# Performance work log

Hardware: AMD Instinct MI355X
Metric: run time of the kernel (lower is better)

Reference implementation:

```python
import jax, jax.numpy as jnp
import numpy as np

B, S, D = 2, 1024, 1024          # batch, seq_len, d_model
L, H = 512, 16                   # latent_d_model, num_heads
HD = L // H                      # latent head dim = 32
F, E, K = 2048, 8, 2             # d_ff per expert, num_experts, top_k
THETA = 10000.0
EPS = 1e-5


def setup_inputs() -> dict:
    key = jax.random.key(0)
    ks = jax.random.split(key, 12)
    g = lambda k, shape, scale: jax.random.normal(k, shape, dtype=jnp.float32) * scale
    return {
        "x": g(ks[0], (B, S, D), 1.0),
        "g1": jnp.ones((D,), jnp.float32),
        "g2": jnp.ones((D,), jnp.float32),
        "w_down": g(ks[1], (D, L), 0.02),   # latent down-projection
        "wq": g(ks[2], (L, L), 0.02),
        "wk": g(ks[3], (L, L), 0.02),
        "wv": g(ks[4], (L, L), 0.02),
        "w_up": g(ks[5], (L, D), 0.02),     # output up-projection
        "router_w": g(ks[6], (D, E), 0.02),
        "w1": g(ks[7], (E, D, F), 0.02),    # SwiGLU gate proj per expert
        "w3": g(ks[8], (E, D, F), 0.02),    # SwiGLU up proj per expert
        "w2": g(ks[9], (E, F, D), 0.02),    # SwiGLU down proj per expert
    }


def _rmsnorm(x, g):
    return x * g * jax.lax.rsqrt(jnp.mean(x * x, axis=-1, keepdims=True) + EPS)


def _rope(t, pos):
    # t: [B, H, S, HD]; RoPE on interleaved pairs of the compressed-latent heads
    inv_freq = 1.0 / (THETA ** (jnp.arange(0, HD, 2, dtype=jnp.float32) / HD))  # [HD/2]
    ang = pos[:, None].astype(jnp.float32) * inv_freq[None, :]                  # [S, HD/2]
    cos, sin = jnp.cos(ang), jnp.sin(ang)
    t1, t2 = t[..., 0::2], t[..., 1::2]
    r1 = t1 * cos - t2 * sin
    r2 = t1 * sin + t2 * cos
    return jnp.stack([r1, r2], axis=-1).reshape(t.shape)


def _forward(x, g1, g2, w_down, wq, wk, wv, w_up, router_w, w1, w2, w3):
    b, s, _ = x.shape
    pos = jnp.arange(s)

    # --- MLA (latent multi-head self-attention with RoPE) ---
    h = _rmsnorm(x, g1)
    c = h @ w_down                                        # [b,s,L] compressed latent
    split = lambda t: t.reshape(b, s, H, HD).transpose(0, 2, 1, 3)
    q = _rope(split(c @ wq), pos)
    k = _rope(split(c @ wk), pos)
    v = split(c @ wv)
    scores = jnp.einsum("bhqd,bhkd->bhqk", q, k) / jnp.sqrt(jnp.float32(HD))
    causal = jnp.tril(jnp.ones((s, s), bool))
    scores = jnp.where(causal, scores, -jnp.inf)
    attn = jax.nn.softmax(scores, axis=-1)
    o = jnp.einsum("bhqk,bhkd->bhqd", attn, v).transpose(0, 2, 1, 3).reshape(b, s, L)
    x = x + o @ w_up

    # --- Switch MoE FFN (top-k routing, SwiGLU experts) ---
    res = x
    t = _rmsnorm(x, g2).reshape(-1, D)                    # [T,D]
    probs = jax.nn.softmax(t @ router_w, axis=-1)         # [T,E]
    vals, idx = jax.lax.top_k(probs, K)                   # [T,K]
    w = vals / jnp.sum(vals, axis=-1, keepdims=True)      # renormalized gates
    gate = jnp.sum(jax.nn.one_hot(idx, E, dtype=t.dtype) * w[..., None], axis=1)  # [T,E]
    hid = jax.nn.silu(jnp.einsum("td,edf->tef", t, w1)) * jnp.einsum("td,edf->tef", t, w3)
    y_e = jnp.einsum("tef,efd->ted", hid, w2)             # per-expert outputs
    y = jnp.einsum("ted,te->td", y_e, gate)
    return res + y.reshape(b, s, D)


def reference(x, g1, g2, w_down, wq, wk, wv, w_up, router_w, w1, w2, w3):
    return _forward(x, g1, g2, w_down, wq, wk, wv, w_up, router_w, w1, w2, w3)
```

## Files before the change

kernel.cpp:

```cpp
#include <hip/hip_runtime.h>

#define Bb 2
#define Ss 1024
#define Dd 1024
#define Ll 512
#define Hh 16
#define HDd 32
#define Ff 2048
#define Ee 8
#define Tt 2048
#define EPSf 1e-5f
#define THETAf 10000.0f

typedef unsigned short u16;
typedef unsigned int u32;
typedef short s16x8 __attribute__((ext_vector_type(8)));
typedef float f32x4 __attribute__((ext_vector_type(4)));

__device__ __forceinline__ float bf2f(u16 u) {
    union { u32 i; float f; } v; v.i = ((u32)u) << 16; return v.f;
}
__device__ __forceinline__ u16 f2bf(float f) {
    union { float f; u32 i; } v; v.f = f;
    u32 u = v.i;
    u32 r = (u + 0x7FFFu + ((u >> 16) & 1u)) >> 16;
    return (u16)r;
}

__global__ __launch_bounds__(256) void rmsnorm1_k(const float* __restrict__ x,
                                                  const float* __restrict__ g,
                                                  u16* __restrict__ hhi,
                                                  u16* __restrict__ hlo) {
    int row = blockIdx.x, tid = threadIdx.x;
    __shared__ float red[256];
    float xv[4]; float ss = 0.f;
    #pragma unroll
    for (int i = 0; i < 4; i++) {
        int d = tid + i * 256;
        xv[i] = x[(size_t)row * Dd + d];
        ss += xv[i] * xv[i];
    }
    red[tid] = ss; __syncthreads();
    for (int s2 = 128; s2 > 0; s2 >>= 1) {
        if (tid < s2) red[tid] += red[tid + s2];
        __syncthreads();
    }
    float scale = rsqrtf(red[0] / (float)Dd + EPSf);
    #pragma unroll
    for (int i = 0; i < 4; i++) {
        int d = tid + i * 256;
        float h = xv[i] * g[d] * scale;
        u16 hi = f2bf(h);
        hhi[(size_t)row * Dd + d] = hi;
        hlo[(size_t)row * Dd + d] = f2bf(h - bf2f(hi));
    }
}

__global__ __launch_bounds__(256) void rmsnorm2_router_k(
    const float* __restrict__ x2, const float* __restrict__ g,
    const float* __restrict__ rw, u16* __restrict__ t2h,
    float* __restrict__ gate_w, int* __restrict__ counts,
    int* __restrict__ list_tok, int* __restrict__ list_gid) {
    int row = blockIdx.x, tid = threadIdx.x;
    __shared__ float red[256];
    __shared__ float pw[4][8];
    float xv[4]; float ss = 0.f;
    #pragma unroll
    for (int i = 0; i < 4; i++) {
        int d = tid + i * 256;
        xv[i] = x2[(size_t)row * Dd + d];
        ss += xv[i] * xv[i];
    }
    red[tid] = ss; __syncthreads();
    for (int s2 = 128; s2 > 0; s2 >>= 1) {
        if (tid < s2) red[tid] += red[tid + s2];
        __syncthreads();
    }
    float scale = rsqrtf(red[0] / (float)Dd + EPSf);
    float pl[Ee];
    #pragma unroll
    for (int e = 0; e < Ee; e++) pl[e] = 0.f;
    #pragma unroll
    for (int i = 0; i < 4; i++) {
        int d = tid + i * 256;
        float h = xv[i] * g[d] * scale;
        t2h[(size_t)row * Dd + d] = f2bf(h);
        const float4* rp = (const float4*)(rw + (size_t)d * Ee);
        float4 r0 = rp[0], r1 = rp[1];
        pl[0] += h * r0.x; pl[1] += h * r0.y; pl[2] += h * r0.z; pl[3] += h * r0.w;
        pl[4] += h * r1.x; pl[5] += h * r1.y; pl[6] += h * r1.z; pl[7] += h * r1.w;
    }
    #pragma unroll
    for (int off = 32; off > 0; off >>= 1) {
        #pragma unroll
        for (int e = 0; e < Ee; e++) pl[e] += __shfl_xor(pl[e], off);
    }
    int wv = tid >> 6;
    if ((tid & 63) == 0) {
        #pragma unroll
        for (int e = 0; e < Ee; e++) pw[wv][e] = pl[e];
    }
    __syncthreads();
    if (tid == 0) {
        float p[Ee];
        #pragma unroll
        for (int e = 0; e < Ee; e++) p[e] = pw[0][e] + pw[1][e] + pw[2][e] + pw[3][e];
        int i0 = 0;
        for (int e = 1; e < Ee; e++) if (p[e] > p[i0]) i0 = e;
        int i1 = (i0 == 0) ? 1 : 0;
        for (int e = 0; e < Ee; e++) if (e != i0 && p[e] > p[i1]) i1 = e;
        float e1 = expf(p[i1] - p[i0]);
        float w0 = 1.f / (1.f + e1), w1 = e1 / (1.f + e1);
        gate_w[2 * row] = w0;
        gate_w[2 * row + 1] = w1;
        int p0 = atomicAdd(&counts[i0], 1);
        list_tok[i0 * Tt + p0] = row;
        list_gid[i0 * Tt + p0] = 2 * row;
        int p1 = atomicAdd(&counts[i1], 1);
        list_tok[i1 * Tt + p1] = row;
        list_gid[i1 * Tt + p1] = 2 * row + 1;
    }
}

template <int SPLITA, int BSPLIT, int GLU, int GATHER, int EPI, int ZM>
__global__ __launch_bounds__(256) void gemm_k(
    const u16* __restrict__ Ah, const u16* __restrict__ Al,
    const float* __restrict__ B1, const float* __restrict__ B3,
    const float* __restrict__ B2,
    int M, int N, int Kd, int lda, int ldb, int ldc, long bzs, long czs,
    const int* __restrict__ arow, const int* __restrict__ crow,
    const int* __restrict__ cntp, const float* __restrict__ gate_f,
    float* __restrict__ Cf, u16* __restrict__ Chi, u16* __restrict__ Clo,
    const float* __restrict__ residf, u16* __restrict__ Cbf) {
    __shared__ __align__(16) u16 As[64 * 40];
    __shared__ __align__(16) u16 Als[64 * 40];
    __shared__ __align__(16) u16 Bs[64 * 40];
    __shared__ __align__(16) u16 Bx[64 * 40];
    int tid = threadIdx.x;
    int row0 = blockIdx.y * 64, col0 = blockIdx.x * 64;
    int z = ZM ? blockIdx.z : 0;
    const float* Bp = B1;
    const float* B3p = B3;
    if (ZM == 1) Bp = (z == 0) ? B1 : ((z == 1) ? B3 : B2);
    if (ZM == 2) {
        Bp = B1 + (size_t)z * bzs;
        if (GLU) B3p = B3 + (size_t)z * bzs;
    }
    const int* arp = arow;
    const int* crp = crow;
    if (ZM == 2 && GATHER) { arp = arow + z * Tt; crp = crow + z * Tt; }
    int cnt = GATHER ? cntp[ZM == 2 ? z : 0] : M;
    if (row0 >= cnt) return;
    float* Cfp = (ZM == 1) ? (Cf + (size_t)z * czs) : Cf;

    int lane = tid & 63, wv = tid >> 6;
    int m = lane & 15, qq = lane >> 4;
    f32x4 acc[4]; f32x4 acc3[4];
    #pragma unroll
    for (int i = 0; i < 4; i++) {
        acc[i] = (f32x4){0.f, 0.f, 0.f, 0.f};
        acc3[i] = (f32x4){0.f, 0.f, 0.f, 0.f};
    }
    int ra = tid >> 2, kca = (tid & 3) * 8;
    int rb = tid >> 3, ncb = (tid & 7) * 8;
    int ar = row0 + ra;
    if (GATHER) ar = arp[min(ar, cnt - 1)];
    const u16* pA = Ah + (size_t)ar * lda + kca;
    const u16* pAl = SPLITA ? (Al + (size_t)ar * lda + kca) : (const u16*)nullptr;
    int cb = rb >> 3;

    for (int k0 = 0; k0 < Kd; k0 += 32) {
        {
            uint4 av = *(const uint4*)(pA + k0);
            *(uint4*)(As + ra * 40 + kca) = av;
            if (SPLITA) {
                uint4 av2 = *(const uint4*)(pAl + k0);
                *(uint4*)(Als + ra * 40 + kca) = av2;
            }
            const float* pB = Bp + (size_t)(k0 + rb) * ldb + col0 + ncb;
            float4 b0 = *(const float4*)pB;
            float4 b1 = *(const float4*)(pB + 4);
            float bb[8] = {b0.x, b0.y, b0.z, b0.w, b1.x, b1.y, b1.z, b1.w};
            #pragma unroll
            for (int j = 0; j < 8; j++) {
                int n = ncb + j;
                int c2 = cb ^ ((n >> 3) & 3);
                int koff = (c2 << 3) | (rb & 7);
                u16 hi = f2bf(bb[j]);
                Bs[n * 40 + koff] = hi;
                if (BSPLIT) Bx[n * 40 + koff] = f2bf(bb[j] - bf2f(hi));
            }
            if (GLU) {
                const float* pB3 = B3p + (size_t)(k0 + rb) * ldb + col0 + ncb;
                float4 c0 = *(const float4*)pB3;
                float4 c1 = *(const float4*)(pB3 + 4);
                float cc[8] = {c0.x, c0.y, c0.z, c0.w, c1.x, c1.y, c1.z, c1.w};
                #pragma unroll
                for (int j = 0; j < 8; j++) {
                    int n = ncb + j;
                    int c2 = cb ^ ((n >> 3) & 3);
                    int koff = (c2 << 3) | (rb & 7);
                    Bx[n * 40 + koff] = f2bf(cc[j]);
                }
            }
        }
        __syncthreads();
        s16x8 af = *(const s16x8*)(As + (wv * 16 + m) * 40 + qq * 8);
        s16x8 al2;
        if (SPLITA) al2 = *(const s16x8*)(Als + (wv * 16 + m) * 40 + qq * 8);
        #pragma unroll
        for (int ct = 0; ct < 4; ct++) {
            int n = ct * 16 + m;
            int c2 = qq ^ ((n >> 3) & 3);
            s16x8 bf = *(const s16x8*)(Bs + n * 40 + c2 * 8);
            acc[ct] = __builtin_amdgcn_mfma_f32_16x16x32_bf16(af, bf, acc[ct], 0, 0, 0);
            if (SPLITA)
                acc[ct] = __builtin_amdgcn_mfma_f32_16x16x32_bf16(al2, bf, acc[ct], 0, 0, 0);
            if (BSPLIT) {
                s16x8 bl = *(const s16x8*)(Bx + n * 40 + c2 * 8);
                acc[ct] = __builtin_amdgcn_mfma_f32_16x16x32_bf16(af, bl, acc[ct], 0, 0, 0);
            }
            if (GLU) {
                s16x8 b3 = *(const s16x8*)(Bx + n * 40 + c2 * 8);
                acc3[ct] = __builtin_amdgcn_mfma_f32_16x16x32_bf16(af, b3, acc3[ct], 0, 0, 0);
            }
        }
        __syncthreads();
    }
    #pragma unroll
    for (int ct = 0; ct < 4; ct++) {
        #pragma unroll
        for (int rg = 0; rg < 4; rg++) {
            int gr = row0 + wv * 16 + qq * 4 + rg;
            int gc = col0 + ct * 16 + m;
            if (GATHER && gr >= cnt) continue;
            float v = acc[ct][rg];
            if (EPI == 4) {
                int gid = crp[gr];
                int tok = gid >> 1;
                atomicAdd(&Cfp[(size_t)tok * ldc + gc], gate_f[gid] * v);
                continue;
            }
            size_t cix;
            if (GATHER) cix = (size_t)crp[gr] * ldc + gc;
            else cix = (size_t)gr * ldc + gc;
            if (EPI == 0) {
                Cfp[cix] = v;
            } else if (EPI == 1) {
                u16 hi = f2bf(v);
                Chi[cix] = hi;
                Clo[cix] = f2bf(v - bf2f(hi));
            } else if (EPI == 2) {
                Cfp[cix] = v + residf[cix];
            } else if (EPI == 3) {
                float sg = v / (1.f + expf(-v));
                Cbf[cix] = f2bf(sg * acc3[ct][rg]);
            }
        }
    }
}

__global__ __launch_bounds__(256) void rope_k(float* __restrict__ q, float* __restrict__ k) {
    int t = blockIdx.x, tid = threadIdx.x;
    int h = tid >> 4, i = tid & 15;
    int pos = t & (Ss - 1);
    float inv = powf(THETAf, -((float)(2 * i)) / (float)HDd);
    float ang = (float)pos * inv;
    float c = cosf(ang), sn = sinf(ang);
    size_t base = (size_t)t * Ll + h * HDd + 2 * i;
    float q1 = q[base], q2 = q[base + 1];
    q[base] = q1 * c - q2 * sn;
    q[base + 1] = q1 * sn + q2 * c;
    float k1 = k[base], k2 = k[base + 1];
    k[base] = k1 * c - k2 * sn;
    k[base + 1] = k1 * sn + k2 * c;
}

__global__ __launch_bounds__(256) void attn_k(const float* __restrict__ qf,
                                              const float* __restrict__ kf,
                                              const float* __restrict__ vf,
                                              u16* __restrict__ ohi, u16* __restrict__ olo) {
    const float SCALE = 0.1767766952966369f;
    int qt = blockIdx.x;
    int bh = blockIdx.y;
    int h = bh & (Hh - 1), b = bh >> 4;
    int tid = threadIdx.x;
    int wv = tid >> 6, lane = tid & 63;
    int m = lane & 15, quad = lane >> 4;

    __shared__ __align__(16) u16 Ksh[64 * 40];
    __shared__ __align__(16) u16 Ksl[64 * 40];
    __shared__ __align__(16) u16 Vsh[32 * 72];
    __shared__ __align__(16) u16 Vsl[32 * 72];
    __shared__ __align__(16) u16 Ph[4][16 * 72];
    __shared__ __align__(16) u16 Pl[4][16 * 72];

    int qrow = qt * 64 + wv * 16 + m;
    const float* qp = qf + (size_t)(b * Ss + qrow) * Ll + h * HDd + quad * 8;
    float4 q0 = *(const float4*)qp;
    float4 q1 = *(const float4*)(qp + 4);
    float qvv[8] = {q0.x, q0.y, q0.z, q0.w, q1.x, q1.y, q1.z, q1.w};
    s16x8 qh, ql;
    #pragma unroll
    for (int j = 0; j < 8; j++) {
        u16 hi = f2bf(qvv[j]);
        qh[j] = (short)hi;
        ql[j] = (short)f2bf(qvv[j] - bf2f(hi));
    }

    float mrun[4], lrun[4];
    f32x4 o0 = (f32x4){0.f, 0.f, 0.f, 0.f};
    f32x4 o1 = (f32x4){0.f, 0.f, 0.f, 0.f};
    #pragma unroll
    for (int rg = 0; rg < 4; rg++) { mrun[rg] = -1e30f; lrun[rg] = 0.f; }

    int skey = tid >> 2, sd0 = (tid & 3) * 8;
    for (int kt = 0; kt <= qt; kt++) {
        int kbase = kt * 64;
        {
            const float* kp = kf + (size_t)(b * Ss + kbase + skey) * Ll + h * HDd + sd0;
            float4 a0 = *(const float4*)kp;
            float4 a1 = *(const float4*)(kp + 4);
            float kvv[8] = {a0.x, a0.y, a0.z, a0.w, a1.x, a1.y, a1.z, a1.w};
            s16x8 khv, klv;
            #pragma unroll
            for (int j = 0; j < 8; j++) {
                u16 hi = f2bf(kvv[j]);
                khv[j] = (short)hi;
                klv[j] = (short)f2bf(kvv[j] - bf2f(hi));
            }
            *(s16x8*)(Ksh + skey * 40 + sd0) = khv;
            *(s16x8*)(Ksl + skey * 40 + sd0) = klv;
            const float* vp = vf + (size_t)(b * Ss + kbase + skey) * Ll + h * HDd + sd0;
            float4 c0 = *(const float4*)vp;
            float4 c1 = *(const float4*)(vp + 4);
            float vvv[8] = {c0.x, c0.y, c0.z, c0.w, c1.x, c1.y, c1.z, c1.w};
            #pragma unroll
            for (int j = 0; j < 8; j++) {
                int d = sd0 + j;
                int c2 = (skey >> 3) ^ ((d >> 3) & 7);
                int koff = (c2 << 3) | (skey & 7);
                u16 hi = f2bf(vvv[j]);
                Vsh[d * 72 + koff] = hi;
                Vsl[d * 72 + koff] = f2bf(vvv[j] - bf2f(hi));
            }
        }
        __syncthreads();
        f32x4 sc[4];
        #pragma unroll
        for (int ct = 0; ct < 4; ct++) {
            int n = ct * 16 + m;
            s16x8 kh = *(const s16x8*)(Ksh + n * 40 + quad * 8);
            s16x8 kl = *(const s16x8*)(Ksl + n * 40 + quad * 8);
            f32x4 a = (f32x4){0.f, 0.f, 0.f, 0.f};
            a = __builtin_amdgcn_mfma_f32_16x16x32_bf16(qh, kh, a, 0, 0, 0);
            a = __builtin_amdgcn_mfma_f32_16x16x32_bf16(ql, kh, a, 0, 0, 0);
            a = __builtin_amdgcn_mfma_f32_16x16x32_bf16(qh, kl, a, 0, 0, 0);
            sc[ct] = a;
        }
        #pragma unroll
        for (int rg = 0; rg < 4; rg++) {
            int qr = qt * 64 + wv * 16 + quad * 4 + rg;
            float s4[4];
            #pragma unroll
            for (int ct = 0; ct < 4; ct++) {
                float sv = sc[ct][rg] * SCALE;
                if (kbase + ct * 16 + m > qr) sv = -1e30f;
                s4[ct] = sv;
            }
            float tm = fmaxf(fmaxf(s4[0], s4[1]), fmaxf(s4[2], s4[3]));
            #pragma unroll
            for (int off = 8; off > 0; off >>= 1) tm = fmaxf(tm, __shfl_xor(tm, off));
            float mnew = fmaxf(mrun[rg], tm);
            float psum = 0.f;
            float p4[4];
            #pragma unroll
            for (int ct = 0; ct < 4; ct++) {
                p4[ct] = expf(s4[ct] - mnew);
                psum += p4[ct];
            }
            #pragma unroll
            for (int off = 8; off > 0; off >>= 1) psum += __shfl_xor(psum, off);
            float alpha = expf(mrun[rg] - mnew);
            mrun[rg] = mnew;
            lrun[rg] = lrun[rg] * alpha + psum;
            o0[rg] *= alpha;
            o1[rg] *= alpha;
            int prow = quad * 4 + rg;
            #pragma unroll
            for (int ct = 0; ct < 4; ct++) {
                u16 hi = f2bf(p4[ct]);
                Ph[wv][prow * 72 + ct * 16 + m] = hi;
                Pl[wv][prow * 72 + ct * 16 + m] = f2bf(p4[ct] - bf2f(hi));
            }
        }
        #pragma unroll
        for (int kc = 0; kc < 2; kc++) {
            s16x8 pah = *(const s16x8*)(Ph[wv] + m * 72 + kc * 32 + quad * 8);
            s16x8 pal = *(const s16x8*)(Pl[wv] + m * 72 + kc * 32 + quad * 8);
            #pragma unroll
            for (int ct = 0; ct < 2; ct++) {
                int d = ct * 16 + m;
                int c2 = (kc * 4 + quad) ^ ((d >> 3) & 7);
                s16x8 vh = *(const s16x8*)(Vsh + d * 72 + c2 * 8);
                s16x8 vl2 = *(const s16x8*)(Vsl + d * 72 + c2 * 8);
                if (ct == 0) {
                    o0 = __builtin_amdgcn_mfma_f32_16x16x32_bf16(pah, vh, o0, 0, 0, 0);
                    o0 = __builtin_amdgcn_mfma_f32_16x16x32_bf16(pal, vh, o0, 0, 0, 0);
                    o0 = __builtin_amdgcn_mfma_f32_16x16x32_bf16(pah, vl2, o0, 0, 0, 0);
                } else {
                    o1 = __builtin_amdgcn_mfma_f32_16x16x32_bf16(pah, vh, o1, 0, 0, 0);
                    o1 = __builtin_amdgcn_mfma_f32_16x16x32_bf16(pal, vh, o1, 0, 0, 0);
                    o1 = __builtin_amdgcn_mfma_f32_16x16x32_bf16(pah, vl2, o1, 0, 0, 0);
                }
            }
        }
        __syncthreads();
    }
    #pragma unroll
    for (int rg = 0; rg < 4; rg++) {
        float inv = 1.f / lrun[rg];
        int tok = b * Ss + qt * 64 + wv * 16 + quad * 4 + rg;
        #pragma unroll
        for (int ct = 0; ct < 2; ct++) {
            float ov = (ct ? o1[rg] : o0[rg]) * inv;
            int d = ct * 16 + m;
            u16 hi = f2bf(ov);
            ohi[(size_t)tok * Ll + h * HDd + d] = hi;
            olo[(size_t)tok * Ll + h * HDd + d] = f2bf(ov - bf2f(hi));
        }
    }
}

__global__ __launch_bounds__(256) void final_k(const float* __restrict__ x2,
                                               float* __restrict__ out) {
    int t = blockIdx.x, tid = threadIdx.x;
    #pragma unroll
    for (int i = 0; i < 4; i++) {
        int d = tid + i * 256;
        size_t ix = (size_t)t * Dd + d;
        out[ix] = out[ix] + x2[ix];
    }
}

extern "C" void kernel_launch(void* const* d_in, const int* in_sizes, int n_in,
                              void* d_out, int out_size, void* d_ws, size_t ws_size,
                              hipStream_t stream) {
    const float* x       = (const float*)d_in[0];
    const float* g1      = (const float*)d_in[1];
    const float* g2      = (const float*)d_in[2];
    const float* w_down  = (const float*)d_in[3];
    const float* wq      = (const float*)d_in[4];
    const float* wk      = (const float*)d_in[5];
    const float* wv      = (const float*)d_in[6];
    const float* w_up    = (const float*)d_in[7];
    const float* rw      = (const float*)d_in[8];
    const float* w1      = (const float*)d_in[9];
    const float* w3      = (const float*)d_in[10];
    const float* w2      = (const float*)d_in[11];
    float* out = (float*)d_out;

    char* S = (char*)d_ws;
    u16*   h_hi = (u16*)(S + (size_t)0);
    u16*   h_lo = (u16*)(S + ((size_t)4 << 20));
    float* qf   = (float*)(S + (size_t)0);
    float* kf   = (float*)(S + ((size_t)4 << 20));
    float* vf   = (float*)(S + ((size_t)8 << 20));
    u16*   o_hi = (u16*)(S + ((size_t)12 << 20));
    u16*   o_lo = (u16*)(S + ((size_t)14 << 20));
    u16*   hid  = (u16*)(S + (size_t)0);
    char* p = (char*)d_ws + ((size_t)16 << 20);
    u16*   c_hi   = (u16*)p;   p += (size_t)Tt * Ll * 2;
    u16*   c_lo   = (u16*)p;   p += (size_t)Tt * Ll * 2;
    u16*   t2h    = (u16*)p;   p += (size_t)Tt * Dd * 2;
    float* x2f    = (float*)p; p += (size_t)Tt * Dd * 4;
    float* gate_w = (float*)p; p += (size_t)Tt * 2 * 4;
    int*   counts = (int*)p;   p += 256;
    int*   l_tok  = (int*)p;   p += (size_t)Ee * Tt * 4;
    int*   l_gid  = (int*)p;   p += (size_t)Ee * Tt * 4;

    hipMemsetAsync(counts, 0, 256, stream);
    hipMemsetAsync(out, 0, (size_t)Tt * Dd * 4, stream);

    rmsnorm1_k<<<Tt, 256, 0, stream>>>(x, g1, h_hi, h_lo);

    gemm_k<1, 1, 0, 0, 1, 0><<<dim3(Ll / 64, Tt / 64), 256, 0, stream>>>(
        h_hi, h_lo, w_down, nullptr, nullptr, Tt, Ll, Dd, Dd, Ll, Ll, 0, 0,
        nullptr, nullptr, nullptr, nullptr, nullptr, c_hi, c_lo, nullptr, nullptr);

    gemm_k<1, 1, 0, 0, 0, 1><<<dim3(Ll / 64, Tt / 64, 3), 256, 0, stream>>>(
        c_hi, c_lo, wq, wk, wv, Tt, Ll, Ll, Ll, Ll, Ll, 0, (long)Tt * Ll,
        nullptr, nullptr, nullptr, nullptr, qf, nullptr, nullptr, nullptr, nullptr);

    rope_k<<<Tt, 256, 0, stream>>>(qf, kf);

    attn_k<<<dim3(Ss / 64, Bb * Hh), 256, 0, stream>>>(qf, kf, vf, o_hi, o_lo);

    gemm_k<1, 1, 0, 0, 2, 0><<<dim3(Dd / 64, Tt / 64), 256, 0, stream>>>(
        o_hi, o_lo, w_up, nullptr, nullptr, Tt, Dd, Ll, Ll, Dd, Dd, 0, 0,
        nullptr, nullptr, nullptr, nullptr, x2f, nullptr, nullptr, x, nullptr);

    rmsnorm2_router_k<<<Tt, 256, 0, stream>>>(x2f, g2, rw, t2h, gate_w,
                                              counts, l_tok, l_gid);

    gemm_k<0, 0, 1, 1, 3, 2><<<dim3(Ff / 64, Tt / 64, Ee), 256, 0, stream>>>(
        t2h, nullptr, w1, w3, nullptr, Tt, Ff, Dd, Dd, Ff, Ff,
        (long)Dd * Ff, 0, l_tok, l_gid, counts, nullptr,
        nullptr, nullptr, nullptr, nullptr, hid);

    gemm_k<0, 0, 0, 1, 4, 2><<<dim3(Dd / 64, Tt / 64, Ee), 256, 0, stream>>>(
        hid, nullptr, w2, nullptr, nullptr, Tt, Dd, Ff, Ff, Dd, Dd,
        (long)Ff * Dd, 0, l_gid, l_gid, counts, gate_w,
        out, nullptr, nullptr, nullptr, nullptr);

    final_k<<<Tt, 256, 0, stream>>>(x2f, out);
}
```

Measured before the change: 645.4 us.

## Generalize GEMM to multi-tile warps with register-prefetched global loads

```diff
diff --git a/kernel.cpp b/kernel.cpp
--- a/kernel.cpp
+++ b/kernel.cpp
@@ -122,7 +122,7 @@
     }
 }
 
-template <int SPLITA, int BSPLIT, int GLU, int GATHER, int EPI, int ZM>
+template <int BMW, int BNW, int SPLIT, int GLU, int GATHER, int EPI, int ZM>
 __global__ __launch_bounds__(256) void gemm_k(
     const u16* __restrict__ Ah, const u16* __restrict__ Al,
     const float* __restrict__ B1, const float* __restrict__ B3,
@@ -132,12 +132,18 @@
     const int* __restrict__ cntp, const float* __restrict__ gate_f,
     float* __restrict__ Cf, u16* __restrict__ Chi, u16* __restrict__ Clo,
     const float* __restrict__ residf, u16* __restrict__ Cbf) {
-    __shared__ __align__(16) u16 As[64 * 40];
-    __shared__ __align__(16) u16 Als[64 * 40];
-    __shared__ __align__(16) u16 Bs[64 * 40];
-    __shared__ __align__(16) u16 Bx[64 * 40];
+    constexpr int BM = 32 * BMW, BN = 32 * BNW;
+    constexpr int AR = BMW / 2;
+    constexpr int BI = BNW / 2;
+    constexpr int TPR = BN / 8;
+    constexpr int STEP = 256 / TPR;
+    __shared__ __align__(16) u16 Ash[BM * 40];
+    __shared__ __align__(16) u16 Asl[SPLIT ? BM * 40 : 8];
+    __shared__ __align__(16) u16 Bsh[BN * 40];
+    __shared__ __align__(16) u16 Bsx[(SPLIT || GLU) ? BN * 40 : 8];
+
     int tid = threadIdx.x;
-    int row0 = blockIdx.y * 64, col0 = blockIdx.x * 64;
+    int row0 = blockIdx.y * BM, col0 = blockIdx.x * BN;
     int z = ZM ? blockIdx.z : 0;
     const float* Bp = B1;
     const float* B3p = B3;
@@ -155,106 +161,154 @@
 
     int lane = tid & 63, wv = tid >> 6;
     int m = lane & 15, qq = lane >> 4;
-    f32x4 acc[4]; f32x4 acc3[4];
-    #pragma unroll
-    for (int i = 0; i < 4; i++) {
-        acc[i] = (f32x4){0.f, 0.f, 0.f, 0.f};
-        acc3[i] = (f32x4){0.f, 0.f, 0.f, 0.f};
-    }
-    int ra = tid >> 2, kca = (tid & 3) * 8;
-    int rb = tid >> 3, ncb = (tid & 7) * 8;
-    int ar = row0 + ra;
-    if (GATHER) ar = arp[min(ar, cnt - 1)];
-    const u16* pA = Ah + (size_t)ar * lda + kca;
-    const u16* pAl = SPLITA ? (Al + (size_t)ar * lda + kca) : (const u16*)nullptr;
-    int cb = rb >> 3;
-
-    for (int k0 = 0; k0 < Kd; k0 += 32) {
-        {
-            uint4 av = *(const uint4*)(pA + k0);
-            *(uint4*)(As + ra * 40 + kca) = av;
-            if (SPLITA) {
-                uint4 av2 = *(const uint4*)(pAl + k0);
-                *(uint4*)(Als + ra * 40 + kca) = av2;
-            }
-            const float* pB = Bp + (size_t)(k0 + rb) * ldb + col0 + ncb;
-            float4 b0 = *(const float4*)pB;
-            float4 b1 = *(const float4*)(pB + 4);
-            float bb[8] = {b0.x, b0.y, b0.z, b0.w, b1.x, b1.y, b1.z, b1.w};
+    int wrow = wv >> 1, wcol = wv & 1;
+    int rbase = wrow * BMW * 16, cbase = wcol * BNW * 16;
+
+    f32x4 acc[BMW][BNW];
+    f32x4 acc3[GLU ? BMW : 1][GLU ? BNW : 1];
+    #pragma unroll
+    for (int i = 0; i < BMW; i++)
+        #pragma unroll
+        for (int j = 0; j < BNW; j++) acc[i][j] = (f32x4){0.f, 0.f, 0.f, 0.f};
+    if (GLU) {
+        #pragma unroll
+        for (int i = 0; i < BMW; i++)
+            #pragma unroll
+            for (int j = 0; j < BNW; j++) acc3[i][j] = (f32x4){0.f, 0.f, 0.f, 0.f};
+    }
+
+    int rak = (tid & 3) * 8;
+    const u16* pA[AR]; const u16* pAl[AR]; int rloc[AR];
+    #pragma unroll
+    for (int i = 0; i < AR; i++) {
+        rloc[i] = i * 64 + (tid >> 2);
+        int ar = row0 + rloc[i];
+        if (GATHER) ar = arp[min(ar, cnt - 1)];
+        pA[i] = Ah + (size_t)ar * lda + rak;
+        if (SPLIT) pAl[i] = Al + (size_t)ar * lda + rak;
+    }
+    int rbl[BI], ncb = (tid % TPR) * 8;
+    #pragma unroll
+    for (int i = 0; i < BI; i++) rbl[i] = i * STEP + tid / TPR;
+
+    uint4 rAh[AR], rAl[SPLIT ? AR : 1];
+    float4 rB[BI][2], rB3[GLU ? BI : 1][2];
+
+    auto loadT = [&](int k0) {
+        #pragma unroll
+        for (int i = 0; i < AR; i++) {
+            rAh[i] = *(const uint4*)(pA[i] + k0);
+            if (SPLIT) rAl[i] = *(const uint4*)(pAl[i] + k0);
+        }
+        #pragma unroll
+        for (int i = 0; i < BI; i++) {
+            const float* pB = Bp + (size_t)(k0 + rbl[i]) * ldb + col0 + ncb;
+            rB[i][0] = *(const float4*)pB;
+            rB[i][1] = *(const float4*)(pB + 4);
+            if (GLU) {
+                const float* pB3 = B3p + (size_t)(k0 + rbl[i]) * ldb + col0 + ncb;
+                rB3[i][0] = *(const float4*)pB3;
+                rB3[i][1] = *(const float4*)(pB3 + 4);
+            }
+        }
+    };
+    auto storeT = [&]() {
+        #pragma unroll
+        for (int i = 0; i < AR; i++) {
+            *(uint4*)(Ash + rloc[i] * 40 + rak) = rAh[i];
+            if (SPLIT) *(uint4*)(Asl + rloc[i] * 40 + rak) = rAl[i];
+        }
+        #pragma unroll
+        for (int i = 0; i < BI; i++) {
+            int rb = rbl[i], cb = rb >> 3, rb7 = rb & 7;
+            float bb[8];
+            *(float4*)&bb[0] = rB[i][0]; *(float4*)&bb[4] = rB[i][1];
             #pragma unroll
             for (int j = 0; j < 8; j++) {
                 int n = ncb + j;
-                int c2 = cb ^ ((n >> 3) & 3);
-                int koff = (c2 << 3) | (rb & 7);
+                int koff = (((cb ^ ((n >> 3) & 3)) << 3) | rb7);
                 u16 hi = f2bf(bb[j]);
-                Bs[n * 40 + koff] = hi;
-                if (BSPLIT) Bx[n * 40 + koff] = f2bf(bb[j] - bf2f(hi));
+                Bsh[n * 40 + koff] = hi;
+                if (SPLIT) Bsx[n * 40 + koff] = f2bf(bb[j] - bf2f(hi));
             }
             if (GLU) {
-                const float* pB3 = B3p + (size_t)(k0 + rb) * ldb + col0 + ncb;
-                float4 c0 = *(const float4*)pB3;
-                float4 c1 = *(const float4*)(pB3 + 4);
-                float cc[8] = {c0.x, c0.y, c0.z, c0.w, c1.x, c1.y, c1.z, c1.w};
+                float cc[8];
+                *(float4*)&cc[0] = rB3[i][0]; *(float4*)&cc[4] = rB3[i][1];
                 #pragma unroll
                 for (int j = 0; j < 8; j++) {
                     int n = ncb + j;
-                    int c2 = cb ^ ((n >> 3) & 3);
-                    int koff = (c2 << 3) | (rb & 7);
-                    Bx[n * 40 + koff] = f2bf(cc[j]);
+                    int koff = (((cb ^ ((n >> 3) & 3)) << 3) | rb7);
+                    Bsx[n * 40 + koff] = f2bf(cc[j]);
                 }
             }
         }
+    };
+
+    loadT(0);
+    int nk = Kd / 32;
+    for (int kc = 0; kc < nk; kc++) {
+        storeT();
         __syncthreads();
-        s16x8 af = *(const s16x8*)(As + (wv * 16 + m) * 40 + qq * 8);
-        s16x8 al2;
-        if (SPLITA) al2 = *(const s16x8*)(Als + (wv * 16 + m) * 40 + qq * 8);
-        #pragma unroll
-        for (int ct = 0; ct < 4; ct++) {
-            int n = ct * 16 + m;
-            int c2 = qq ^ ((n >> 3) & 3);
-            s16x8 bf = *(const s16x8*)(Bs + n * 40 + c2 * 8);
-            acc[ct] = __builtin_amdgcn_mfma_f32_16x16x32_bf16(af, bf, acc[ct], 0, 0, 0);
-            if (SPLITA)
-                acc[ct] = __builtin_amdgcn_mfma_f32_16x16x32_bf16(al2, bf, acc[ct], 0, 0, 0);
-            if (BSPLIT) {
-                s16x8 bl = *(const s16x8*)(Bx + n * 40 + c2 * 8);
-                acc[ct] = __builtin_amdgcn_mfma_f32_16x16x32_bf16(af, bl, acc[ct], 0, 0, 0);
-            }
-            if (GLU) {
-                s16x8 b3 = *(const s16x8*)(Bx + n * 40 + c2 * 8);
-                acc3[ct] = __builtin_amdgcn_mfma_f32_16x16x32_bf16(af, b3, acc3[ct], 0, 0, 0);
+        if (kc + 1 < nk) loadT((kc + 1) * 32);
+        s16x8 afh[BMW], afl[SPLIT ? BMW : 1], bfh[BNW], bfx[(SPLIT || GLU) ? BNW : 1];
+        #pragma unroll
+        for (int mt = 0; mt < BMW; mt++) {
+            int off = (rbase + mt * 16 + m) * 40 + qq * 8;
+            afh[mt] = *(const s16x8*)(Ash + off);
+            if (SPLIT) afl[mt] = *(const s16x8*)(Asl + off);
+        }
+        #pragma unroll
+        for (int ct = 0; ct < BNW; ct++) {
+            int n = cbase + ct * 16 + m;
+            int off = n * 40 + (qq ^ ((n >> 3) & 3)) * 8;
+            bfh[ct] = *(const s16x8*)(Bsh + off);
+            if (SPLIT || GLU) bfx[ct] = *(const s16x8*)(Bsx + off);
+        }
+        #pragma unroll
+        for (int mt = 0; mt < BMW; mt++) {
+            #pragma unroll
+            for (int ct = 0; ct < BNW; ct++) {
+                acc[mt][ct] = __builtin_amdgcn_mfma_f32_16x16x32_bf16(afh[mt], bfh[ct], acc[mt][ct], 0, 0, 0);
+                if (SPLIT) {
+                    acc[mt][ct] = __builtin_amdgcn_mfma_f32_16x16x32_bf16(afl[mt], bfh[ct], acc[mt][ct], 0, 0, 0);
+                    acc[mt][ct] = __builtin_amdgcn_mfma_f32_16x16x32_bf16(afh[mt], bfx[ct], acc[mt][ct], 0, 0, 0);
+                }
+                if (GLU)
+                    acc3[mt][ct] = __builtin_amdgcn_mfma_f32_16x16x32_bf16(afh[mt], bfx[ct], acc3[mt][ct], 0, 0, 0);
             }
         }
         __syncthreads();
     }
     #pragma unroll
-    for (int ct = 0; ct < 4; ct++) {
-        #pragma unroll
-        for (int rg = 0; rg < 4; rg++) {
-            int gr = row0 + wv * 16 + qq * 4 + rg;
-            int gc = col0 + ct * 16 + m;
-            if (GATHER && gr >= cnt) continue;
-            float v = acc[ct][rg];
-            if (EPI == 4) {
-                int gid = crp[gr];
-                int tok = gid >> 1;
-                atomicAdd(&Cfp[(size_t)tok * ldc + gc], gate_f[gid] * v);
-                continue;
-            }
-            size_t cix;
-            if (GATHER) cix = (size_t)crp[gr] * ldc + gc;
-            else cix = (size_t)gr * ldc + gc;
-            if (EPI == 0) {
-                Cfp[cix] = v;
-            } else if (EPI == 1) {
-                u16 hi = f2bf(v);
-                Chi[cix] = hi;
-                Clo[cix] = f2bf(v - bf2f(hi));
-            } else if (EPI == 2) {
-                Cfp[cix] = v + residf[cix];
-            } else if (EPI == 3) {
-                float sg = v / (1.f + expf(-v));
-                Cbf[cix] = f2bf(sg * acc3[ct][rg]);
+    for (int mt = 0; mt < BMW; mt++) {
+        #pragma unroll
+        for (int ct = 0; ct < BNW; ct++) {
+            #pragma unroll
+            for (int rg = 0; rg < 4; rg++) {
+                int gr = row0 + rbase + mt * 16 + qq * 4 + rg;
+                int gc = col0 + cbase + ct * 16 + m;
+                if (GATHER && gr >= cnt) continue;
+                float v = acc[mt][ct][rg];
+                if (EPI == 4) {
+                    int gid = crp[gr];
+                    atomicAdd(&Cfp[(size_t)(gid >> 1) * ldc + gc], gate_f[gid] * v);
+                    continue;
+                }
+                size_t cix;
+                if (GATHER) cix = (size_t)crp[gr] * ldc + gc;
+                else cix = (size_t)gr * ldc + gc;
+                if (EPI == 0) {
+                    Cfp[cix] = v;
+                } else if (EPI == 1) {
+                    u16 hi = f2bf(v);
+                    Chi[cix] = hi;
+                    Clo[cix] = f2bf(v - bf2f(hi));
+                } else if (EPI == 2) {
+                    Cfp[cix] = v + residf[cix];
+                } else if (EPI == 3) {
+                    float sg = v / (1.f + expf(-v));
+                    Cbf[cix] = f2bf(sg * acc3[mt][ct][rg]);
+                }
             }
         }
     }
@@ -484,11 +538,11 @@
 
     rmsnorm1_k<<<Tt, 256, 0, stream>>>(x, g1, h_hi, h_lo);
 
-    gemm_k<1, 1, 0, 0, 1, 0><<<dim3(Ll / 64, Tt / 64), 256, 0, stream>>>(
+    gemm_k<2, 2, 1, 0, 0, 1, 0><<<dim3(Ll / 64, Tt / 64), 256, 0, stream>>>(
         h_hi, h_lo, w_down, nullptr, nullptr, Tt, Ll, Dd, Dd, Ll, Ll, 0, 0,
         nullptr, nullptr, nullptr, nullptr, nullptr, c_hi, c_lo, nullptr, nullptr);
 
-    gemm_k<1, 1, 0, 0, 0, 1><<<dim3(Ll / 64, Tt / 64, 3), 256, 0, stream>>>(
+    gemm_k<2, 2, 1, 0, 0, 0, 1><<<dim3(Ll / 64, Tt / 64, 3), 256, 0, stream>>>(
         c_hi, c_lo, wq, wk, wv, Tt, Ll, Ll, Ll, Ll, Ll, 0, (long)Tt * Ll,
         nullptr, nullptr, nullptr, nullptr, qf, nullptr, nullptr, nullptr, nullptr);
 
@@ -496,19 +550,19 @@
 
     attn_k<<<dim3(Ss / 64, Bb * Hh), 256, 0, stream>>>(qf, kf, vf, o_hi, o_lo);
 
-    gemm_k<1, 1, 0, 0, 2, 0><<<dim3(Dd / 64, Tt / 64), 256, 0, stream>>>(
+    gemm_k<2, 2, 1, 0, 0, 2, 0><<<dim3(Dd / 64, Tt / 64), 256, 0, stream>>>(
         o_hi, o_lo, w_up, nullptr, nullptr, Tt, Dd, Ll, Ll, Dd, Dd, 0, 0,
         nullptr, nullptr, nullptr, nullptr, x2f, nullptr, nullptr, x, nullptr);
 
     rmsnorm2_router_k<<<Tt, 256, 0, stream>>>(x2f, g2, rw, t2h, gate_w,
                                               counts, l_tok, l_gid);
 
-    gemm_k<0, 0, 1, 1, 3, 2><<<dim3(Ff / 64, Tt / 64, Ee), 256, 0, stream>>>(
+    gemm_k<4, 2, 0, 1, 1, 3, 2><<<dim3(Ff / 64, Tt / 128, Ee), 256, 0, stream>>>(
         t2h, nullptr, w1, w3, nullptr, Tt, Ff, Dd, Dd, Ff, Ff,
         (long)Dd * Ff, 0, l_tok, l_gid, counts, nullptr,
         nullptr, nullptr, nullptr, nullptr, hid);
 
-    gemm_k<0, 0, 0, 1, 4, 2><<<dim3(Dd / 64, Tt / 64, Ee), 256, 0, stream>>>(
+    gemm_k<4, 4, 0, 0, 1, 4, 2><<<dim3(Dd / 128, Tt / 128, Ee), 256, 0, stream>>>(
         hid, nullptr, w2, nullptr, nullptr, Tt, Dd, Ff, Ff, Dd, Dd,
         (long)Ff * Dd, 0, l_gid, l_gid, counts, gate_w,
         out, nullptr, nullptr, nullptr, nullptr);
```

Result: slower. 734.0 us (+13.7%).
